# Performance work log

Measured on AMD Instinct MI355X. Metric: run time of the kernel, lower is better.

Reference implementation:

```python
import jax, jax.numpy as jnp
import numpy as np

EMB, GCN = 256, 256
N_REL = 200
B, E, TOPK = 256, 100000, 64
N_PREV, N_ENT, N_TIME = 50000, 20000, 2000


def _linear(x, w, b):
    # torch nn.Linear convention: w is [out, in]
    return x @ w.T + b


def setup_inputs() -> dict:
    key = jax.random.key(0)
    ks = jax.random.split(key, 32)
    nrm = lambda k, s: (jax.random.normal(k, s, jnp.float32) * 0.05)
    # facts columns: b, n, h, r, t, ts. b built so every batch has >= TOPK facts.
    b_col = jax.random.permutation(ks[0], jnp.arange(E, dtype=jnp.int32) % B)
    n_col = jax.random.randint(ks[1], (E,), 0, N_PREV, jnp.int32)
    h_col = jax.random.randint(ks[2], (E,), 0, N_ENT, jnp.int32)
    r_col = jax.random.randint(ks[3], (E,), 0, N_REL, jnp.int32)  # r+1 indexes [zero;rel]
    t_col = jax.random.randint(ks[4], (E,), 0, N_ENT, jnp.int32)
    ts_col = jax.random.randint(ks[5], (E,), 0, N_TIME, jnp.int32)
    facts = jnp.stack([b_col, n_col, h_col, r_col, t_col, ts_col], axis=1)
    return {
        "query_time": jax.random.randint(ks[6], (B,), 0, N_TIME, jnp.int32),  # unused by forward
        "query_emd": nrm(ks[7], (B, EMB)),
        "temp_neighbors_facts": facts,
        "ent_emd": nrm(ks[8], (N_ENT, GCN)),
        "rel_emd": nrm(ks[9], (N_REL, GCN)),
        "hidden_node": nrm(ks[10], (N_PREV, EMB)),
        "hidden_rel": nrm(ks[11], (N_PREV, EMB)),
        "hidden_time": nrm(ks[12], (N_PREV, EMB)),  # unused by forward
        "att_agg": jax.random.uniform(ks[13], (N_PREV,), jnp.float32),
        "time_emd": nrm(ks[14], (N_TIME, EMB)),
        "zero_rel_emd": nrm(ks[15], (1, GCN)),
        "W_message_w": nrm(ks[16], (EMB, 2 * EMB)), "W_message_b": jnp.zeros((EMB,), jnp.float32),
        "att_1_w": nrm(ks[17], (1, 3 * EMB)), "att_1_b": jnp.zeros((1,), jnp.float32),
        "att_2_w": nrm(ks[18], (1, EMB)), "att_2_b": jnp.zeros((1,), jnp.float32),
        "W_h_w": nrm(ks[19], (EMB, 2 * EMB)), "W_h_b": jnp.zeros((EMB,), jnp.float32),
        "lin_e_ts_w": nrm(ks[20], (EMB, GCN + EMB)), "lin_e_ts_b": jnp.zeros((EMB,), jnp.float32),
        "lin_r_ts_w": nrm(ks[21], (EMB, GCN)), "lin_r_ts_b": jnp.zeros((EMB,), jnp.float32),
        "lin_time_w": nrm(ks[22], (EMB, EMB)), "lin_time_b": jnp.zeros((EMB,), jnp.float32),
        "gru_w_ih": nrm(ks[23], (3 * EMB, EMB)), "gru_w_hh": nrm(ks[24], (3 * EMB, EMB)),
        "gru_b_ih": jnp.zeros((3 * EMB,), jnp.float32), "gru_b_hh": jnp.zeros((3 * EMB,), jnp.float32),
        "batch_size": B, "device": 0, "max_nodes": TOPK,
    }


def reference(query_time, query_emd, temp_neighbors_facts, ent_emd, rel_emd,
              hidden_node, hidden_rel, hidden_time, att_agg, time_emd,
              zero_rel_emd, W_message_w, W_message_b, att_1_w, att_1_b,
              att_2_w, att_2_b, W_h_w, W_h_b, lin_e_ts_w, lin_e_ts_b,
              lin_r_ts_w, lin_r_ts_b, lin_time_w, lin_time_b,
              gru_w_ih, gru_w_hh, gru_b_ih, gru_b_hh,
              batch_size, device, max_nodes):
    f = temp_neighbors_facts
    b, n, r, t, ts = f[:, 0], f[:, 1], f[:, 3], f[:, 4], f[:, 5]

    hidden_node_pre = hidden_node[n]            # [E, EMB]
    hidden_rel_pre = hidden_rel[n]              # [E, EMB]
    rel_all = jnp.concatenate([zero_rel_emd, rel_emd], axis=0)
    h_r = rel_all[r + 1]                        # [E, GCN]
    h_ts_raw = time_emd[ts]                     # [E, EMB]
    h_t = _linear(jnp.concatenate([ent_emd[t], h_ts_raw], -1), lin_e_ts_w, lin_e_ts_b)
    h_r = _linear(h_r, lin_r_ts_w, lin_r_ts_b)
    _ = _linear(h_ts_raw, lin_time_w, lin_time_b)  # computed but unused in original

    message = _linear(jnp.concatenate([hidden_node_pre, h_r], -1), W_message_w, W_message_b)
    att_input = jnp.concatenate([query_emd[b], message, h_t], -1)  # [E, 3*EMB]
    att1 = jax.nn.sigmoid(_linear(att_input, att_1_w, att_1_b))[:, 0]

    # single-step GRU (torch nn.GRU gate math)
    gi = h_r @ gru_w_ih.T + gru_b_ih            # [E, 3*EMB]
    gh = hidden_rel_pre @ gru_w_hh.T + gru_b_hh
    i_r, i_z, i_n = jnp.split(gi, 3, axis=-1)
    h_rg, h_zg, h_ng = jnp.split(gh, 3, axis=-1)
    rg = jax.nn.sigmoid(i_r + h_rg)
    zg = jax.nn.sigmoid(i_z + h_zg)
    ng = jnp.tanh(i_n + rg * h_ng)
    hidden_rel_new = (1.0 - zg) * ng + zg * hidden_rel_pre

    att2 = jax.nn.sigmoid(_linear(hidden_rel_new, att_2_w, att_2_b))[:, 0]
    attention = (att1 + att2) * 0.5

    # vectorized per-batch top-k (each batch is guaranteed >= max_nodes facts)
    order = jnp.lexsort((-attention, b))        # sort by batch asc, attention desc
    counts = jax.ops.segment_sum(jnp.ones_like(b), b, num_segments=batch_size)
    starts = jnp.cumsum(counts) - counts
    sel = (starts[:, None] + jnp.arange(max_nodes)[None, :]).reshape(-1)
    new_index = order[sel]                      # [B*topk]

    facts_k = f[new_index]
    message = message[new_index]
    hidden_rel_new = hidden_rel_new[new_index]
    attention = (att1[new_index] + att2[new_index]) * 0.5
    b_k, n_k = facts_k[:, 0], facts_k[:, 1]
    attention = attention * att_agg[n_k]
    M = b_k.shape[0]

    rows = facts_k[:, jnp.array([0, 4, 5])]     # (b, t, ts)
    tail_nodes, tail_index = jnp.unique(rows, axis=0, size=M, fill_value=0, return_inverse=True)
    tail_index = tail_index.reshape(-1)

    tail_emd = _linear(jnp.concatenate([ent_emd[tail_nodes[:, 1]], time_emd[tail_nodes[:, 2]]], -1),
                       lin_e_ts_w, lin_e_ts_b)

    # group_max_norm: normalize attention by per-batch sum (0/0 -> 0)
    den = jax.ops.segment_sum(attention, b_k, num_segments=batch_size)[b_k]
    safe_den = jnp.where(den != 0, den, 1.0)
    attention = jnp.where(den != 0, attention / safe_den, 0.0)

    message_agg = jax.ops.segment_sum(attention[:, None] * message, tail_index, num_segments=M)
    hidden_node_new = _linear(jnp.concatenate([message_agg, tail_emd], -1), W_h_w, W_h_b)  # act = identity
    hidden_rel_out = jax.ops.segment_sum(attention[:, None] * hidden_rel_new, tail_index, num_segments=M)
    att_agg_new = jax.ops.segment_sum(attention, tail_index, num_segments=M)
    return tail_nodes, hidden_node_new, hidden_rel_out, att_agg_new
```

## Files before the change

kernel.cpp:

```cpp
#include <hip/hip_runtime.h>
#include <hip/hip_bf16.h>

#define E_N    100000
#define B_N    256
#define TOPK   64
#define NPREV  50000
#define NENT   20000
#define NTIME  2000
#define NREL   200
#define M_OUT  16384
#define NT8    6250

static __device__ __forceinline__ float sigm(float x){ return 1.f/(1.f+expf(-x)); }

__global__ void zero_kernel(unsigned* __restrict__ p, int n){
  int i = blockIdx.x*256 + threadIdx.x;
  if (i < n) p[i] = 0u;
}

__global__ void pack_w_kernel(const float* __restrict__ w_msg,
                              const float* __restrict__ w_hh,
                              const float* __restrict__ lets_w,
                              const float* __restrict__ w_h,
                              float4* __restrict__ wP,
                              float4* __restrict__ wPL,
                              float4* __restrict__ wPH){
  int i = blockIdx.x*256 + threadIdx.x;
  if (i < 65536){
    int t = i & 255, mat = (i >> 8) & 3, kblk = i >> 10;
    float4 v;
    if (mat == 0) v = *(const float4*)&w_msg[(size_t)t*512 + kblk*4];
    else          v = *(const float4*)&w_hh[(size_t)((mat-1)*256 + t)*256 + kblk*4];
    wP[i] = v;
  } else if (i < 98304){
    int j = i - 65536;
    int t = j & 255, mat = (j >> 8) & 1, kblk = j >> 9;
    wPL[j] = *(const float4*)&lets_w[(size_t)t*512 + mat*256 + kblk*4];
  } else if (i < 131072){
    int j = i - 98304;
    int t = j & 255, kblk = j >> 8;
    wPH[j] = *(const float4*)&w_h[(size_t)t*512 + kblk*4];
  }
}

__global__ void matvec_fused(const float* __restrict__ w_msg,
                             const float* __restrict__ lets_w,
                             const float* __restrict__ lets_b,
                             const float* __restrict__ att1w,
                             const float* __restrict__ att1b,
                             float* __restrict__ wm1a, float* __restrict__ ve,
                             float* __restrict__ vts, float* __restrict__ consts){
  int blk = blockIdx.x, t = threadIdx.x;
  if (blk == 3){
    if (t < 64){
      float p = 0.f;
      for (int d = t; d < 256; d += 64) p += lets_b[d]*att1w[512+d];
      for (int o = 32; o > 0; o >>= 1) p += __shfl_down(p, o);
      if (t == 0) consts[0] = att1b[0] + p;
    }
    return;
  }
  const float* M; int moff; const float* v; float* out;
  if (blk == 0){ M = w_msg;  moff = 0;   v = att1w+256; out = wm1a; }
  else if (blk == 1){ M = lets_w; moff = 0;   v = att1w+512; out = ve; }
  else { M = lets_w; moff = 256; v = att1w+512; out = vts; }
  float acc = 0.f;
  for (int d = 0; d < 256; ++d) acc += M[(size_t)d*512 + moff + t] * v[d];
  out[t] = acc;
}

__global__ void rows_dot_multi(
    const float* __restrict__ A0, const float* __restrict__ v0, float* __restrict__ o0, int n0,
    const float* __restrict__ A1, const float* __restrict__ v1, float* __restrict__ o1_, int n1,
    const float* __restrict__ A2, const float* __restrict__ v2, float* __restrict__ o2, int n2,
    const float* __restrict__ A3, const float* __restrict__ v3, float* __restrict__ o3, int n3,
    const float* __restrict__ A4, const float* __restrict__ v4, float* __restrict__ o4, int n4){
  int gid = blockIdx.x*256 + threadIdx.x;
  int wid = gid >> 6, lane = gid & 63;
  const float* A; const float* v; float* o; int r;
  if (wid < n0){ A=A0; v=v0; o=o0; r=wid; }
  else if ((wid -= n0) < n1){ A=A1; v=v1; o=o1_; r=wid; }
  else if ((wid -= n1) < n2){ A=A2; v=v2; o=o2; r=wid; }
  else if ((wid -= n2) < n3){ A=A3; v=v3; o=o3; r=wid; }
  else if ((wid -= n3) < n4){ A=A4; v=v4; o=o4; r=wid; }
  else return;
  const float* row = A + (size_t)r*256;
  float p = 0.f;
  for (int k = lane; k < 256; k += 64) p += row[k]*v[k];
  for (int off = 32; off > 0; off >>= 1) p += __shfl_down(p, off);
  if (lane == 0) o[r] = p;
}

template<int ND>
__global__ __launch_bounds__(256) void tile_linear(
    const float* __restrict__ A, int lda,
    const float* __restrict__ Bw, int ldb, int boff,
    const float* __restrict__ bias,
    float* __restrict__ out, int ldo, int rows){
  __shared__ float a_s[16][260];
  int tile0 = blockIdx.x*16;
  for (int idx = threadIdx.x; idx < 16*256; idx += 256){
    int i = idx >> 8, k = idx & 255;
    int row = tile0 + i;
    a_s[i][k] = (row < rows) ? A[(size_t)row*lda + k] : 0.f;
  }
  __syncthreads();
  int d = threadIdx.x;
  const float* brow[ND];
  #pragma unroll
  for (int q = 0; q < ND; ++q) brow[q] = Bw + (size_t)(d + 256*q)*ldb + boff;
  float acc[ND][16];
  #pragma unroll
  for (int q = 0; q < ND; ++q){
    float bv = bias ? bias[d + 256*q] : 0.f;
    #pragma unroll
    for (int i = 0; i < 16; ++i) acc[q][i] = bv;
  }
  for (int k = 0; k < 256; k += 4){
    float4 w[ND];
    #pragma unroll
    for (int q = 0; q < ND; ++q) w[q] = *(const float4*)(brow[q] + k);
    #pragma unroll
    for (int i = 0; i < 16; ++i){
      float4 a = *(const float4*)&a_s[i][k];
      #pragma unroll
      for (int q = 0; q < ND; ++q)
        acc[q][i] += w[q].x*a.x + w[q].y*a.y + w[q].z*a.z + w[q].w*a.w;
    }
  }
  #pragma unroll
  for (int i = 0; i < 16; ++i){
    int row = tile0 + i;
    if (row < rows){
      #pragma unroll
      for (int q = 0; q < ND; ++q) out[(size_t)row*ldo + d + 256*q] = acc[q][i];
    }
  }
}

__global__ __launch_bounds__(256) void gemv_ets(
    const float* __restrict__ act, const float4* __restrict__ wPL, int matsel,
    const float* __restrict__ bias, float* __restrict__ out){
  int tile0 = blockIdx.x*16, t = threadIdx.x;
  float acc[16];
  float bv = bias ? bias[t] : 0.f;
  #pragma unroll
  for (int p = 0; p < 16; ++p) acc[p] = bv;
  float4 w = wPL[matsel*256 + t];
  for (int kb = 0; kb < 64; ++kb){
    int kbn = (kb + 1) & 63;
    float4 nw = wPL[(kbn*2 + matsel)*256 + t];
    int k = kb*4;
    #pragma unroll
    for (int p = 0; p < 16; ++p){
      float4 a = *(const float4*)&act[(size_t)(tile0+p)*256 + k];
      acc[p] += w.x*a.x + w.y*a.y + w.z*a.z + w.w*a.w;
    }
    w = nw;
  }
  #pragma unroll
  for (int p = 0; p < 16; ++p)
    out[(size_t)(tile0+p)*256 + t] = acc[p];
}

__global__ void hist2_kernel(const int* __restrict__ facts,
                             int* __restrict__ cnt_t, int* __restrict__ cnt_b){
  int e = blockIdx.x*256 + threadIdx.x;
  if (e < E_N){
    atomicAdd(&cnt_t[facts[e*6+1] >> 3], 1);
    atomicAdd(&cnt_b[facts[e*6+0]], 1);
  }
}

__global__ void scan2_kernel(const int* __restrict__ cnt_t, int* __restrict__ off_t, int* __restrict__ cur_t,
                             const int* __restrict__ cnt_b, int* __restrict__ off_b, int* __restrict__ cur_b){
  const int* cnt; int* off; int* cur; int n;
  if (blockIdx.x == 0){ cnt = cnt_t; off = off_t; cur = cur_t; n = NT8; }
  else { cnt = cnt_b; off = off_b; cur = cur_b; n = B_N; }
  int lane = threadIdx.x;
  int run = 0;
  int npad = (n + 63) & ~63;
  for (int base = 0; base < npad; base += 64){
    int idx = base + lane;
    int orig = (idx < n) ? cnt[idx] : 0;
    int v = orig;
    for (int o = 1; o < 64; o <<= 1){ int t = __shfl_up(v, o); if (lane >= o) v += t; }
    if (idx < n){ int ex = run + v - orig; off[idx] = ex; cur[idx] = ex; }
    run += __shfl(v, 63);
  }
  if (lane == 0) off[n] = E_N;
}

__global__ void scatter2_kernel(const int* __restrict__ facts,
                                int* __restrict__ cur_t, int* __restrict__ edges_t,
                                int* __restrict__ cur_b, int* __restrict__ edges_b){
  int e = blockIdx.x*256 + threadIdx.x;
  if (e < E_N){
    int pt = atomicAdd(&cur_t[facts[e*6+1] >> 3], 1);
    edges_t[pt] = e;
    int pb = atomicAdd(&cur_b[facts[e*6+0]], 1);
    edges_b[pb] = e;
  }
}

__global__ __launch_bounds__(256) void att_kernel(
    const float* __restrict__ hidden_rel,
    const float4* __restrict__ wP,
    const float* __restrict__ b_hh,
    const float* __restrict__ gi,
    const float* __restrict__ att2w, const float* __restrict__ att2b,
    const int* __restrict__ facts,
    const int* __restrict__ bin_off, const int* __restrict__ bin_edges,
    const float* __restrict__ qdot, const float* __restrict__ sn_m,
    const float* __restrict__ sr_m, const float* __restrict__ se,
    const float* __restrict__ st,   const float* __restrict__ consts,
    float* __restrict__ attention){
  __shared__ float gh_s[8][776];
  int tile0 = blockIdx.x*8;
  int t = threadIdx.x;

  float acc[3][8];
  #pragma unroll
  for (int q = 0; q < 3; ++q)
    #pragma unroll
    for (int p = 0; p < 8; ++p) acc[q][p] = 0.f;

  float4 w1 = wP[256 + t], w2 = wP[512 + t], w3 = wP[768 + t];
  for (int kb = 0; kb < 64; ++kb){
    int kbn = (kb + 1) & 63;
    int nb = (kbn*4)*256 + t;
    float4 nw1 = wP[nb + 256], nw2 = wP[nb + 512], nw3 = wP[nb + 768];
    int k = kb*4;
    #pragma unroll
    for (int p = 0; p < 8; ++p){
      float4 a = *(const float4*)&hidden_rel[(size_t)(tile0+p)*256 + k];
      acc[0][p] += w1.x*a.x + w1.y*a.y + w1.z*a.z + w1.w*a.w;
      acc[1][p] += w2.x*a.x + w2.y*a.y + w2.z*a.z + w2.w*a.w;
      acc[2][p] += w3.x*a.x + w3.y*a.y + w3.z*a.z + w3.w*a.w;
    }
    w1 = nw1; w2 = nw2; w3 = nw3;
  }
  #pragma unroll
  for (int q = 0; q < 3; ++q){
    float bv = b_hh[t + 256*q];
    #pragma unroll
    for (int p = 0; p < 8; ++p)
      gh_s[p][t + 256*q] = acc[q][p] + bv;
  }
  __syncthreads();

  int wv = t >> 6, l = t & 63;
  int o0 = bin_off[blockIdx.x], o1 = bin_off[blockIdx.x + 1];
  int d0 = 4*l;
  float4 a2 = *(const float4*)&att2w[d0];
  float c1 = consts[0];
  float a2b = att2b[0];
  for (int idx = o0 + wv; idx < o1; idx += 4){
    int e  = bin_edges[idx];
    int b  = facts[e*6+0], n = facts[e*6+1], r = facts[e*6+3];
    int t_ = facts[e*6+4], ts_ = facts[e*6+5];
    int nl = n - tile0;
    float4 ghr = *(const float4*)&gh_s[nl][d0];
    float4 ghz = *(const float4*)&gh_s[nl][256+d0];
    float4 ghn = *(const float4*)&gh_s[nl][512+d0];
    const float* girow = gi + (size_t)r*768;
    float4 gir = *(const float4*)&girow[d0];
    float4 giz = *(const float4*)&girow[256+d0];
    float4 gin = *(const float4*)&girow[512+d0];
    float4 hp  = *(const float4*)&hidden_rel[(size_t)n*256 + d0];
    float partial;
    {
      float rg = sigm(gir.x + ghr.x), zg = sigm(giz.x + ghz.x);
      float ng = tanhf(gin.x + rg*ghn.x);
      partial = a2.x * ((1.f - zg)*ng + zg*hp.x);
    }{
      float rg = sigm(gir.y + ghr.y), zg = sigm(giz.y + ghz.y);
      float ng = tanhf(gin.y + rg*ghn.y);
      partial += a2.y * ((1.f - zg)*ng + zg*hp.y);
    }{
      float rg = sigm(gir.z + ghr.z), zg = sigm(giz.z + ghz.z);
      float ng = tanhf(gin.z + rg*ghn.z);
      partial += a2.z * ((1.f - zg)*ng + zg*hp.z);
    }{
      float rg = sigm(gir.w + ghr.w), zg = sigm(giz.w + ghz.w);
      float ng = tanhf(gin.w + rg*ghn.w);
      partial += a2.w * ((1.f - zg)*ng + zg*hp.w);
    }
    #pragma unroll
    for (int o = 32; o > 0; o >>= 1) partial += __shfl_xor(partial, o);
    if (l == 0){
      float att2 = sigm(partial + a2b);
      float x1 = qdot[b] + sn_m[n] + sr_m[r] + se[t_] + st[ts_] + c1;
      attention[e] = 0.5f*(sigm(x1) + att2);
    }
  }
}

__global__ __launch_bounds__(256) void topk_kernel(
    const int* __restrict__ facts, const float* __restrict__ attention,
    const float* __restrict__ att_agg,
    const int* __restrict__ boff, const int* __restrict__ bedges,
    int* __restrict__ sel_edge, float* __restrict__ att_norm,
    unsigned* __restrict__ skey, int* __restrict__ Ub){
  __shared__ float sa[512];
  __shared__ int   si[512];
  __shared__ unsigned sk[64];
  int b = blockIdx.x, tid = threadIdx.x;
  sa[tid] = -1.f; sa[tid+256] = -1.f;
  si[tid] = 0x7fffffff; si[tid+256] = 0x7fffffff;
  __syncthreads();
  int o0 = boff[b], cnt = boff[b+1] - o0;
  for (int i = tid; i < cnt; i += 256){
    int e = bedges[o0 + i];
    sa[i] = attention[e]; si[i] = e;
  }
  __syncthreads();
  for (int k = 2; k <= 512; k <<= 1){
    for (int j = k >> 1; j > 0; j >>= 1){
      for (int i0 = tid; i0 < 512; i0 += 256){
        int l = i0 ^ j;
        if (l > i0){
          float ai = sa[i0], al = sa[l];
          int   ii = si[i0], il = si[l];
          bool lFirst = (al > ai) || (al == ai && il < ii);
          bool up = ((i0 & k) == 0);
          if (up ? lFirst : !lFirst){
            sa[i0] = al; sa[l] = ai; si[i0] = il; si[l] = ii;
          }
        }
      }
      __syncthreads();
    }
  }
  if (tid < 64){
    int e = si[tid];
    bool valid = (e != 0x7fffffff);
    if (!valid) e = 0;
    int n = facts[e*6+1];
    float a = valid ? sa[tid]*att_agg[n] : 0.f;
    float den = a;
    for (int o = 32; o > 0; o >>= 1) den += __shfl_down(den, o);
    den = __shfl(den, 0);
    float norm = (den != 0.f) ? a/den : 0.f;
    sel_edge[b*64 + tid] = e;
    att_norm[b*64 + tid] = norm;
    int t_ = facts[e*6+4], ts_ = facts[e*6+5];
    unsigned key = (((unsigned)t_) << 11) | (unsigned)ts_;
    sk[tid] = (key << 6) | (unsigned)tid;
  }
  __syncthreads();
  for (int k = 2; k <= 64; k <<= 1){
    for (int j = k >> 1; j > 0; j >>= 1){
      unsigned nv = 0; bool act = tid < 64;
      if (act){
        unsigned mine = sk[tid], other = sk[tid ^ j];
        bool up = ((tid & k) == 0);
        bool keepmin = (up == ((tid & j) == 0));
        nv = keepmin ? (mine < other ? mine : other) : (mine > other ? mine : other);
      }
      __syncthreads();
      if (act) sk[tid] = nv;
      __syncthreads();
    }
  }
  if (tid < 64){
    unsigned kk = sk[tid];
    skey[b*64 + tid] = kk;
    bool head = (tid == 0) || ((kk >> 6) != (sk[tid-1] >> 6));
    unsigned long long bal = __ballot(head);
    if (tid == 0) Ub[b] = __popcll(bal);
  }
}

__global__ void offs_scan_kernel(const int* __restrict__ Ub, int* __restrict__ offs){
  int lane = threadIdx.x;
  int run = 0;
  for (int base = 0; base < 256; base += 64){
    int orig = Ub[base + lane];
    int v = orig;
    for (int o = 1; o < 64; o <<= 1){ int t = __shfl_up(v, o); if (lane >= o) v += t; }
    offs[base + lane] = run + v - orig;
    run += __shfl(v, 63);
  }
  if (lane == 0) offs[256] = run;
}

__global__ void emit_kernel(const unsigned* __restrict__ skey, const int* __restrict__ offs,
                            int* __restrict__ us, int* __restrict__ tails,
                            float* __restrict__ out_tail){
  int b = blockIdx.x, tid = threadIdx.x;
  unsigned kk = skey[b*64 + tid];
  bool head = (tid == 0) || ((kk >> 6) != (skey[b*64 + tid - 1] >> 6));
  unsigned long long bal = __ballot(head);
  unsigned long long mask_le = (tid == 63) ? ~0ull : ((1ull << (tid+1)) - 1ull);
  int ulocal = __popcll(bal & mask_le) - 1;
  int u = offs[b] + ulocal;
  us[b*64 + tid] = u;
  if (head){
    unsigned key = kk >> 6;
    int t_ = (int)(key >> 11), ts_ = (int)(key & 2047u);
    tails[u*3+0] = b; tails[u*3+1] = t_; tails[u*3+2] = ts_;
    out_tail[u*3+0] = (float)b;
    out_tail[u*3+1] = (float)t_;
    out_tail[u*3+2] = (float)ts_;
  }
}

__global__ __launch_bounds__(256) void sel_kernel(
    const unsigned* __restrict__ skey, const int* __restrict__ sel_edge,
    const float* __restrict__ att_norm, const int* __restrict__ facts,
    const float* __restrict__ hidden_node, const float* __restrict__ hidden_rel,
    const float4* __restrict__ wP,
    const float* __restrict__ msg_r, const float* __restrict__ gi,
    const float* __restrict__ b_hh,
    float* __restrict__ msg_sel, float* __restrict__ hrn_sel){
  __shared__ int n_s[8], r_s[8];
  __shared__ float av_s[8];
  int base = blockIdx.x*8;
  int t = threadIdx.x;
  if (t < 8){
    int gs = base + t;
    int b = gs >> 6, i = gs & 63;
    int j = (int)(skey[(size_t)b*64 + i] & 63u);
    int s = b*64 + j;
    int e = sel_edge[s];
    n_s[t] = facts[e*6+1];
    r_s[t] = facts[e*6+3];
    av_s[t] = att_norm[s];
  }
  __syncthreads();

  float acc[4][8];
  #pragma unroll
  for (int q = 0; q < 4; ++q)
    #pragma unroll
    for (int e = 0; e < 8; ++e) acc[q][e] = 0.f;

  float4 w0 = wP[t], w1 = wP[256 + t], w2 = wP[512 + t], w3 = wP[768 + t];
  for (int kb = 0; kb < 64; ++kb){
    int kbn = (kb + 1) & 63;
    int nb = (kbn*4)*256 + t;
    float4 nw0 = wP[nb], nw1 = wP[nb + 256], nw2 = wP[nb + 512], nw3 = wP[nb + 768];
    int k = kb*4;
    #pragma unroll
    for (int e = 0; e < 8; ++e){
      float4 an = *(const float4*)&hidden_node[(size_t)n_s[e]*256 + k];
      float4 ah = *(const float4*)&hidden_rel[(size_t)n_s[e]*256 + k];
      acc[0][e] += w0.x*an.x + w0.y*an.y + w0.z*an.z + w0.w*an.w;
      acc[1][e] += w1.x*ah.x + w1.y*ah.y + w1.z*ah.z + w1.w*ah.w;
      acc[2][e] += w2.x*ah.x + w2.y*ah.y + w2.z*ah.z + w2.w*ah.w;
      acc[3][e] += w3.x*ah.x + w3.y*ah.y + w3.z*ah.z + w3.w*ah.w;
    }
    w0 = nw0; w1 = nw1; w2 = nw2; w3 = nw3;
  }

  float bhr = b_hh[t], bhz = b_hh[256+t], bhn = b_hh[512+t];
  #pragma unroll
  for (int e = 0; e < 8; ++e){
    int r = r_s[e]; float a = av_s[e];
    const float* girow = gi + (size_t)r*768;
    float msgv = acc[0][e] + msg_r[(size_t)r*256 + t];
    float rg = sigm(girow[t]      + acc[1][e] + bhr);
    float zg = sigm(girow[256+t]  + acc[2][e] + bhz);
    float ng = tanhf(girow[512+t] + rg*(acc[3][e] + bhn));
    float hp = hidden_rel[(size_t)n_s[e]*256 + t];
    float hrn = (1.f - zg)*ng + zg*hp;
    size_t o = (size_t)(base + e)*256 + t;
    msg_sel[o] = a*msgv;
    hrn_sel[o] = a*hrn;
  }
}

__global__ __launch_bounds__(256) void segsum_kernel(
    const unsigned* __restrict__ skey, const int* __restrict__ us,
    const float* __restrict__ att_norm,
    const float* __restrict__ msg_sel, const float* __restrict__ hrn_sel,
    float* __restrict__ msg_agg, float* __restrict__ out_hrel,
    float* __restrict__ out_aagg){
  int b = blockIdx.x, d = threadIdx.x;
  float accm = 0.f, acch = 0.f, acca = 0.f;
  int ucur = -1;
  for (int i = 0; i < 64; ++i){
    int u = us[b*64 + i];
    if (u != ucur){
      if (ucur >= 0){
        msg_agg[(size_t)ucur*256 + d] = accm;
        out_hrel[(size_t)ucur*256 + d] = acch;
        if (d == 0) out_aagg[ucur] = acca;
      }
      ucur = u; accm = 0.f; acch = 0.f; acca = 0.f;
    }
    size_t o = (size_t)(b*64 + i)*256 + d;
    accm += msg_sel[o];
    acch += hrn_sel[o];
    int j = (int)(skey[b*64 + i] & 63u);
    acca += att_norm[b*64 + j];
  }
  if (ucur >= 0){
    msg_agg[(size_t)ucur*256 + d] = accm;
    out_hrel[(size_t)ucur*256 + d] = acch;
    if (d == 0) out_aagg[ucur] = acca;
  }
}

__global__ __launch_bounds__(256) void final_kernel(
    const float* __restrict__ msg_agg, const int* __restrict__ tails,
    const float* __restrict__ ent_t, const float* __restrict__ time_t,
    const float4* __restrict__ wPH,
    const float* __restrict__ b_h,
    float* __restrict__ out_hn){
  int tile0 = blockIdx.x*16, t = threadIdx.x;
  int tu[16], tsu[16];
  #pragma unroll
  for (int p = 0; p < 16; ++p){
    tu[p]  = tails[(tile0+p)*3+1];
    tsu[p] = tails[(tile0+p)*3+2];
  }
  float acc[16];
  float bv = b_h[t];
  #pragma unroll
  for (int p = 0; p < 16; ++p) acc[p] = bv;
  float4 w = wPH[t];
  for (int kb = 0; kb < 128; ++kb){
    int kbn = (kb + 1) & 127;
    float4 nw = wPH[kbn*256 + t];
    if (kb < 64){
      int k = kb*4;
      #pragma unroll
      for (int p = 0; p < 16; ++p){
        float4 a = *(const float4*)&msg_agg[(size_t)(tile0+p)*256 + k];
        acc[p] += w.x*a.x + w.y*a.y + w.z*a.z + w.w*a.w;
      }
    } else {
      int k = (kb-64)*4;
      #pragma unroll
      for (int p = 0; p < 16; ++p){
        float4 a1 = *(const float4*)&ent_t[(size_t)tu[p]*256 + k];
        float4 a2 = *(const float4*)&time_t[(size_t)tsu[p]*256 + k];
        float ax = a1.x + a2.x, ay = a1.y + a2.y, az = a1.z + a2.z, aw = a1.w + a2.w;
        acc[p] += w.x*ax + w.y*ay + w.z*az + w.w*aw;
      }
    }
    w = nw;
  }
  #pragma unroll
  for (int p = 0; p < 16; ++p)
    out_hn[(size_t)(tile0+p)*256 + t] = acc[p];
}

extern "C" void kernel_launch(void* const* d_in, const int* in_sizes, int n_in,
                              void* d_out, int out_size, void* d_ws, size_t ws_size,
                              hipStream_t stream){
  const float* query_emd   = (const float*)d_in[1];
  const int*   facts       = (const int*)  d_in[2];
  const float* ent_emd     = (const float*)d_in[3];
  const float* rel_emd     = (const float*)d_in[4];
  const float* hidden_node = (const float*)d_in[5];
  const float* hidden_rel  = (const float*)d_in[6];
  const float* att_agg     = (const float*)d_in[8];
  const float* time_emd    = (const float*)d_in[9];
  const float* w_msg       = (const float*)d_in[11];
  const float* b_msg       = (const float*)d_in[12];
  const float* att1w       = (const float*)d_in[13];
  const float* att1b       = (const float*)d_in[14];
  const float* att2w       = (const float*)d_in[15];
  const float* att2b       = (const float*)d_in[16];
  const float* w_h         = (const float*)d_in[17];
  const float* b_h         = (const float*)d_in[18];
  const float* lets_w      = (const float*)d_in[19];
  const float* lets_b      = (const float*)d_in[20];
  const float* lrts_w      = (const float*)d_in[21];
  const float* lrts_b      = (const float*)d_in[22];
  const float* w_ih        = (const float*)d_in[25];
  const float* w_hh        = (const float*)d_in[26];
  const float* b_ih        = (const float*)d_in[27];
  const float* b_hh        = (const float*)d_in[28];

  char* p = (char*)d_ws;
  auto alloc = [&](size_t bytes) -> void* {
    void* r = (void*)p; p += (bytes + 255) & ~(size_t)255; return r;
  };
  char* zstart = p;
  int* bin_cnt  = (int*)alloc(6272*4);
  int* bin_cur  = (int*)alloc(6272*4);
  int* bcnt     = (int*)alloc(256*4);
  int* bcur     = (int*)alloc(256*4);
  int* tails    = (int*)alloc((size_t)M_OUT*3*4);
  float* msg_agg= (float*)alloc((size_t)M_OUT*256*4);
  size_t zero_words = (size_t)(p - zstart)/4;
  int* bin_off  = (int*)alloc(6272*4);
  int* bin_edges= (int*)alloc(E_N*4);
  int* boff     = (int*)alloc(257*4);
  int* bedges   = (int*)alloc(E_N*4);
  float* attention = (float*)alloc(E_N*4);
  float* qdot   = (float*)alloc(256*4);
  float* sn_m   = (float*)alloc(NPREV*4);
  float* se     = (float*)alloc(NENT*4);
  float* st     = (float*)alloc(NTIME*4);
  float* sr_m   = (float*)alloc(NREL*4);
  float* wm1a   = (float*)alloc(256*4);
  float* ve     = (float*)alloc(256*4);
  float* vts    = (float*)alloc(256*4);
  float* consts = (float*)alloc(8*4);
  float* hr2    = (float*)alloc((size_t)NREL*256*4);
  float* msg_r  = (float*)alloc((size_t)NREL*256*4);
  float* gi     = (float*)alloc((size_t)NREL*768*4);
  float* time_t = (float*)alloc((size_t)NTIME*256*4);
  float* ent_t  = (float*)alloc((size_t)NENT*256*4);
  float4* wP    = (float4*)alloc((size_t)65536*16);
  float4* wPL   = (float4*)alloc((size_t)32768*16);
  float4* wPH   = (float4*)alloc((size_t)32768*16);
  int* sel_edge = (int*)alloc(M_OUT*4);
  float* att_nrm= (float*)alloc(M_OUT*4);
  unsigned* skey= (unsigned*)alloc(M_OUT*4);
  int* Ub       = (int*)alloc(256*4);
  int* offs     = (int*)alloc(257*4);
  int* us       = (int*)alloc(M_OUT*4);
  float* msg_sel= (float*)alloc((size_t)M_OUT*256*4);
  float* hrn_sel= (float*)alloc((size_t)M_OUT*256*4);
  (void)ws_size; (void)in_sizes; (void)n_in;

  float* out_f     = (float*)d_out;
  float* out_tail  = out_f;
  float* out_hn    = out_f + (size_t)M_OUT*3;
  float* out_hrel  = out_f + (size_t)M_OUT*3 + (size_t)M_OUT*256;
  float* out_aagg  = out_f + (size_t)M_OUT*3 + (size_t)2*M_OUT*256;

  zero_kernel<<<(out_size+255)/256, 256, 0, stream>>>((unsigned*)d_out, out_size);
  zero_kernel<<<((int)zero_words+255)/256, 256, 0, stream>>>((unsigned*)zstart, (int)zero_words);

  pack_w_kernel<<<512, 256, 0, stream>>>(w_msg, w_hh, lets_w, w_h, wP, wPL, wPH);
  matvec_fused<<<4, 256, 0, stream>>>(w_msg, lets_w, lets_b, att1w, att1b, wm1a, ve, vts, consts);

  tile_linear<1><<<(NREL+15)/16, 256, 0, stream>>>(rel_emd, 256, lrts_w, 256, 0, lrts_b, hr2, 256, NREL);
  tile_linear<1><<<(NREL+15)/16, 256, 0, stream>>>(hr2, 256, w_msg, 512, 256, b_msg, msg_r, 256, NREL);
  tile_linear<3><<<(NREL+15)/16, 256, 0, stream>>>(hr2, 256, w_ih, 256, 0, b_ih, gi, 768, NREL);

  gemv_ets<<<NENT/16, 256, 0, stream>>>(ent_emd, wPL, 0, lets_b, ent_t);
  gemv_ets<<<NTIME/16, 256, 0, stream>>>(time_emd, wPL, 1, (const float*)nullptr, time_t);

  {
    int total_rows = B_N + NPREV + NENT + NTIME + NREL;
    int blocks = (total_rows*64 + 255)/256;
    rows_dot_multi<<<blocks, 256, 0, stream>>>(
        query_emd, att1w, qdot, B_N,
        hidden_node, wm1a, sn_m, NPREV,
        ent_emd, ve, se, NENT,
        time_emd, vts, st, NTIME,
        msg_r, att1w+256, sr_m, NREL);
  }

  hist2_kernel<<<(E_N+255)/256, 256, 0, stream>>>(facts, bin_cnt, bcnt);
  scan2_kernel<<<2, 64, 0, stream>>>(bin_cnt, bin_off, bin_cur, bcnt, boff, bcur);
  scatter2_kernel<<<(E_N+255)/256, 256, 0, stream>>>(facts, bin_cur, bin_edges, bcur, bedges);

  att_kernel<<<NT8, 256, 0, stream>>>(hidden_rel, wP, b_hh, gi, att2w, att2b,
      facts, bin_off, bin_edges, qdot, sn_m, sr_m, se, st, consts, attention);

  topk_kernel<<<B_N, 256, 0, stream>>>(facts, attention, att_agg, boff, bedges,
      sel_edge, att_nrm, skey, Ub);
  offs_scan_kernel<<<1, 64, 0, stream>>>(Ub, offs);
  emit_kernel<<<B_N, 64, 0, stream>>>(skey, offs, us, tails, out_tail);
  sel_kernel<<<M_OUT/8, 256, 0, stream>>>(skey, sel_edge, att_nrm, facts,
      hidden_node, hidden_rel, wP, msg_r, gi, b_hh, msg_sel, hrn_sel);
  segsum_kernel<<<B_N, 256, 0, stream>>>(skey, us, att_nrm, msg_sel, hrn_sel,
      msg_agg, out_hrel, out_aagg);
  final_kernel<<<M_OUT/16, 256, 0, stream>>>(msg_agg, tails, ent_t, time_t, wPH, b_h, out_hn);
}
```

Before: 1.264 ms.

## Enlarge row tiles in gemv_ets and sel_kernel, replace scan with LDS block scan

gemv_ets now handles 64 rows per block instead of 16 and clamps rows at the edge. sel_kernel handles 32 selected edges per block instead of 8. Both changes reuse each loaded weight float4 across more rows, cutting weight re-reads. The two-wave serial scan is replaced by a single 256-thread block scan that uses LDS, and one matvec loop is unrolled. Workspace buffers are reordered. The risks are heavy register pressure from 64 or 128 accumulators per thread, possible spilling, and fewer blocks to fill the GPU.

```diff
diff --git a/kernel.cpp b/kernel.cpp
--- a/kernel.cpp
+++ b/kernel.cpp
@@ -65,6 +65,7 @@
   else if (blk == 1){ M = lets_w; moff = 0;   v = att1w+512; out = ve; }
   else { M = lets_w; moff = 256; v = att1w+512; out = vts; }
   float acc = 0.f;
+  #pragma unroll 8
   for (int d = 0; d < 256; ++d) acc += M[(size_t)d*512 + moff + t] * v[d];
   out[t] = acc;
 }
@@ -140,27 +141,30 @@
 
 __global__ __launch_bounds__(256) void gemv_ets(
     const float* __restrict__ act, const float4* __restrict__ wPL, int matsel,
-    const float* __restrict__ bias, float* __restrict__ out){
-  int tile0 = blockIdx.x*16, t = threadIdx.x;
-  float acc[16];
+    const float* __restrict__ bias, float* __restrict__ out, int rows){
+  int tile0 = blockIdx.x*64, t = threadIdx.x;
+  float acc[64];
   float bv = bias ? bias[t] : 0.f;
   #pragma unroll
-  for (int p = 0; p < 16; ++p) acc[p] = bv;
+  for (int p = 0; p < 64; ++p) acc[p] = bv;
   float4 w = wPL[matsel*256 + t];
   for (int kb = 0; kb < 64; ++kb){
     int kbn = (kb + 1) & 63;
     float4 nw = wPL[(kbn*2 + matsel)*256 + t];
     int k = kb*4;
     #pragma unroll
-    for (int p = 0; p < 16; ++p){
-      float4 a = *(const float4*)&act[(size_t)(tile0+p)*256 + k];
+    for (int p = 0; p < 64; ++p){
+      int row = tile0 + p; if (row > rows-1) row = rows-1;
+      float4 a = *(const float4*)&act[(size_t)row*256 + k];
       acc[p] += w.x*a.x + w.y*a.y + w.z*a.z + w.w*a.w;
     }
     w = nw;
   }
   #pragma unroll
-  for (int p = 0; p < 16; ++p)
-    out[(size_t)(tile0+p)*256 + t] = acc[p];
+  for (int p = 0; p < 64; ++p){
+    int row = tile0 + p;
+    if (row < rows) out[(size_t)row*256 + t] = acc[p];
+  }
 }
 
 __global__ void hist2_kernel(const int* __restrict__ facts,
@@ -172,23 +176,39 @@
   }
 }
 
-__global__ void scan2_kernel(const int* __restrict__ cnt_t, int* __restrict__ off_t, int* __restrict__ cur_t,
-                             const int* __restrict__ cnt_b, int* __restrict__ off_b, int* __restrict__ cur_b){
-  const int* cnt; int* off; int* cur; int n;
-  if (blockIdx.x == 0){ cnt = cnt_t; off = off_t; cur = cur_t; n = NT8; }
-  else { cnt = cnt_b; off = off_b; cur = cur_b; n = B_N; }
-  int lane = threadIdx.x;
-  int run = 0;
-  int npad = (n + 63) & ~63;
-  for (int base = 0; base < npad; base += 64){
-    int idx = base + lane;
-    int orig = (idx < n) ? cnt[idx] : 0;
-    int v = orig;
-    for (int o = 1; o < 64; o <<= 1){ int t = __shfl_up(v, o); if (lane >= o) v += t; }
-    if (idx < n){ int ex = run + v - orig; off[idx] = ex; cur[idx] = ex; }
-    run += __shfl(v, 63);
-  }
-  if (lane == 0) off[n] = E_N;
+__global__ __launch_bounds__(256) void scan2_lds(
+    const int* __restrict__ cnt_t, int* __restrict__ off_t, int* __restrict__ cur_t,
+    const int* __restrict__ cnt_b, int* __restrict__ off_b, int* __restrict__ cur_b){
+  __shared__ int buf[6272];
+  __shared__ int sums[256];
+  int t = threadIdx.x;
+  int c0 = t*25, c1 = c0 + 25; if (c1 > NT8) c1 = NT8; if (c0 > NT8) c0 = NT8;
+  int s = 0;
+  for (int i = c0; i < c1; ++i){ buf[i] = s; s += cnt_t[i]; }
+  sums[t] = s;
+  __syncthreads();
+  for (int o = 1; o < 256; o <<= 1){
+    int v = (t >= o) ? sums[t-o] : 0;
+    __syncthreads();
+    sums[t] += v;
+    __syncthreads();
+  }
+  int add = (t == 0) ? 0 : sums[t-1];
+  for (int i = c0; i < c1; ++i){ int v = buf[i] + add; off_t[i] = v; cur_t[i] = v; }
+  if (t == 0) off_t[NT8] = E_N;
+  __syncthreads();
+  int orig = cnt_b[t];
+  sums[t] = orig;
+  __syncthreads();
+  for (int o = 1; o < 256; o <<= 1){
+    int v = (t >= o) ? sums[t-o] : 0;
+    __syncthreads();
+    sums[t] += v;
+    __syncthreads();
+  }
+  int ex = sums[t] - orig;
+  off_b[t] = ex; cur_b[t] = ex;
+  if (t == 0) off_b[B_N] = E_N;
 }
 
 __global__ void scatter2_kernel(const int* __restrict__ facts,
@@ -414,11 +434,11 @@
     const float* __restrict__ msg_r, const float* __restrict__ gi,
     const float* __restrict__ b_hh,
     float* __restrict__ msg_sel, float* __restrict__ hrn_sel){
-  __shared__ int n_s[8], r_s[8];
-  __shared__ float av_s[8];
-  int base = blockIdx.x*8;
+  __shared__ int n_s[32], r_s[32];
+  __shared__ float av_s[32];
+  int base = blockIdx.x*32;
   int t = threadIdx.x;
-  if (t < 8){
+  if (t < 32){
     int gs = base + t;
     int b = gs >> 6, i = gs & 63;
     int j = (int)(skey[(size_t)b*64 + i] & 63u);
@@ -430,11 +450,9 @@
   }
   __syncthreads();
 
-  float acc[4][8];
-  #pragma unroll
-  for (int q = 0; q < 4; ++q)
-    #pragma unroll
-    for (int e = 0; e < 8; ++e) acc[q][e] = 0.f;
+  float accM[32], accR[32], accZ[32], accN[32];
+  #pragma unroll
+  for (int e = 0; e < 32; ++e){ accM[e]=0.f; accR[e]=0.f; accZ[e]=0.f; accN[e]=0.f; }
 
   float4 w0 = wP[t], w1 = wP[256 + t], w2 = wP[512 + t], w3 = wP[768 + t];
   for (int kb = 0; kb < 64; ++kb){
@@ -443,26 +461,26 @@
     float4 nw0 = wP[nb], nw1 = wP[nb + 256], nw2 = wP[nb + 512], nw3 = wP[nb + 768];
     int k = kb*4;
     #pragma unroll
-    for (int e = 0; e < 8; ++e){
+    for (int e = 0; e < 32; ++e){
       float4 an = *(const float4*)&hidden_node[(size_t)n_s[e]*256 + k];
       float4 ah = *(const float4*)&hidden_rel[(size_t)n_s[e]*256 + k];
-      acc[0][e] += w0.x*an.x + w0.y*an.y + w0.z*an.z + w0.w*an.w;
-      acc[1][e] += w1.x*ah.x + w1.y*ah.y + w1.z*ah.z + w1.w*ah.w;
-      acc[2][e] += w2.x*ah.x + w2.y*ah.y + w2.z*ah.z + w2.w*ah.w;
-      acc[3][e] += w3.x*ah.x + w3.y*ah.y + w3.z*ah.z + w3.w*ah.w;
+      accM[e] += w0.x*an.x + w0.y*an.y + w0.z*an.z + w0.w*an.w;
+      accR[e] += w1.x*ah.x + w1.y*ah.y + w1.z*ah.z + w1.w*ah.w;
+      accZ[e] += w2.x*ah.x + w2.y*ah.y + w2.z*ah.z + w2.w*ah.w;
+      accN[e] += w3.x*ah.x + w3.y*ah.y + w3.z*ah.z + w3.w*ah.w;
     }
     w0 = nw0; w1 = nw1; w2 = nw2; w3 = nw3;
   }
 
   float bhr = b_hh[t], bhz = b_hh[256+t], bhn = b_hh[512+t];
   #pragma unroll
-  for (int e = 0; e < 8; ++e){
+  for (int e = 0; e < 32; ++e){
     int r = r_s[e]; float a = av_s[e];
     const float* girow = gi + (size_t)r*768;
-    float msgv = acc[0][e] + msg_r[(size_t)r*256 + t];
-    float rg = sigm(girow[t]      + acc[1][e] + bhr);
-    float zg = sigm(girow[256+t]  + acc[2][e] + bhz);
-    float ng = tanhf(girow[512+t] + rg*(acc[3][e] + bhn));
+    float msgv = accM[e] + msg_r[(size_t)r*256 + t];
+    float rg = sigm(girow[t]      + accR[e] + bhr);
+    float zg = sigm(girow[256+t]  + accZ[e] + bhz);
+    float ng = tanhf(girow[512+t] + rg*(accN[e] + bhn));
     float hp = hidden_rel[(size_t)n_s[e]*256 + t];
     float hrn = (1.f - zg)*ng + zg*hp;
     size_t o = (size_t)(base + e)*256 + t;
@@ -588,6 +606,10 @@
   int* tails    = (int*)alloc((size_t)M_OUT*3*4);
   float* msg_agg= (float*)alloc((size_t)M_OUT*256*4);
   size_t zero_words = (size_t)(p - zstart)/4;
+  float* msg_sel= (float*)alloc((size_t)M_OUT*256*4);
+  float* hrn_sel= (float*)alloc((size_t)M_OUT*256*4);
+  float* ent_t  = (float*)alloc((size_t)NENT*256*4);
+  float* time_t = (float*)alloc((size_t)NTIME*256*4);
   int* bin_off  = (int*)alloc(6272*4);
   int* bin_edges= (int*)alloc(E_N*4);
   int* boff     = (int*)alloc(257*4);
@@ -605,8 +627,6 @@
   float* hr2    = (float*)alloc((size_t)NREL*256*4);
   float* msg_r  = (float*)alloc((size_t)NREL*256*4);
   float* gi     = (float*)alloc((size_t)NREL*768*4);
-  float* time_t = (float*)alloc((size_t)NTIME*256*4);
-  float* ent_t  = (float*)alloc((size_t)NENT*256*4);
   float4* wP    = (float4*)alloc((size_t)65536*16);
   float4* wPL   = (float4*)alloc((size_t)32768*16);
   float4* wPH   = (float4*)alloc((size_t)32768*16);
@@ -616,8 +636,6 @@
   int* Ub       = (int*)alloc(256*4);
   int* offs     = (int*)alloc(257*4);
   int* us       = (int*)alloc(M_OUT*4);
-  float* msg_sel= (float*)alloc((size_t)M_OUT*256*4);
-  float* hrn_sel= (float*)alloc((size_t)M_OUT*256*4);
   (void)ws_size; (void)in_sizes; (void)n_in;
 
   float* out_f     = (float*)d_out;
@@ -636,8 +654,8 @@
   tile_linear<1><<<(NREL+15)/16, 256, 0, stream>>>(hr2, 256, w_msg, 512, 256, b_msg, msg_r, 256, NREL);
   tile_linear<3><<<(NREL+15)/16, 256, 0, stream>>>(hr2, 256, w_ih, 256, 0, b_ih, gi, 768, NREL);
 
-  gemv_ets<<<NENT/16, 256, 0, stream>>>(ent_emd, wPL, 0, lets_b, ent_t);
-  gemv_ets<<<NTIME/16, 256, 0, stream>>>(time_emd, wPL, 1, (const float*)nullptr, time_t);
+  gemv_ets<<<(NENT+63)/64, 256, 0, stream>>>(ent_emd, wPL, 0, lets_b, ent_t, NENT);
+  gemv_ets<<<(NTIME+63)/64, 256, 0, stream>>>(time_emd, wPL, 1, (const float*)nullptr, time_t, NTIME);
 
   {
     int total_rows = B_N + NPREV + NENT + NTIME + NREL;
@@ -651,7 +669,7 @@
   }
 
   hist2_kernel<<<(E_N+255)/256, 256, 0, stream>>>(facts, bin_cnt, bcnt);
-  scan2_kernel<<<2, 64, 0, stream>>>(bin_cnt, bin_off, bin_cur, bcnt, boff, bcur);
+  scan2_lds<<<1, 256, 0, stream>>>(bin_cnt, bin_off, bin_cur, bcnt, boff, bcur);
   scatter2_kernel<<<(E_N+255)/256, 256, 0, stream>>>(facts, bin_cur, bin_edges, bcur, bedges);
 
   att_kernel<<<NT8, 256, 0, stream>>>(hidden_rel, wP, b_hh, gi, att2w, att2b,
@@ -661,7 +679,7 @@
       sel_edge, att_nrm, skey, Ub);
   offs_scan_kernel<<<1, 64, 0, stream>>>(Ub, offs);
   emit_kernel<<<B_N, 64, 0, stream>>>(skey, offs, us, tails, out_tail);
-  sel_kernel<<<M_OUT/8, 256, 0, stream>>>(skey, sel_edge, att_nrm, facts,
+  sel_kernel<<<M_OUT/32, 256, 0, stream>>>(skey, sel_edge, att_nrm, facts,
       hidden_node, hidden_rel, wP, msg_r, gi, b_hh, msg_sel, hrn_sel);
   segsum_kernel<<<B_N, 256, 0, stream>>>(skey, us, att_nrm, msg_sel, hrn_sel,
       msg_agg, out_hrel, out_aagg);
```

New measurement: 1.975 ms. 1.56x slower.
